# Kernel tuning notes

Hardware: AMD Instinct MI355X
Metric: run time of the kernel (lower is better)

The kernel has to match this reference:

```python
import math
import jax, jax.numpy as jnp
import numpy as np

B, S, D = 4, 2048, 1280
H, HD = 16, 80  # num_heads, head_dim
LOG2E = 1.442695041


def setup_inputs() -> dict:
    key = jax.random.key(0)
    ks = jax.random.split(key, 6)
    hidden_states = jax.random.normal(ks[0], (B, S, D), dtype=jnp.float32)
    # additive causal mask: 0 on/below diagonal, large negative above
    causal = jnp.tril(jnp.ones((S, S), dtype=bool))
    attention_mask = jnp.where(causal, 0.0, -1e9).astype(jnp.float32)[None, None, :, :]
    attention_mask = jnp.broadcast_to(attention_mask, (B, 1, S, S))
    scaling = jax.random.normal(ks[1], (HD,), dtype=jnp.float32)
    fan = 1.0 / math.sqrt(D)
    qkv_w = jax.random.normal(ks[2], (3 * H * HD, D), dtype=jnp.float32) * fan
    qkv_b = jax.random.normal(ks[3], (3 * H * HD,), dtype=jnp.float32) * fan
    o_w = jax.random.normal(ks[4], (D, H * HD), dtype=jnp.float32) * (1.0 / math.sqrt(H * HD))
    o_b = jax.random.normal(ks[5], (D,), dtype=jnp.float32) * fan
    return {
        "hidden_states": hidden_states,
        "attention_mask": attention_mask,
        "scaling": scaling,
        "qkv_w": qkv_w,
        "qkv_b": qkv_b,
        "o_w": o_w,
        "o_b": o_b,
    }


def reference(hidden_states, attention_mask, scaling, qkv_w, qkv_b, o_w, o_b):
    b, s, _ = hidden_states.shape
    qkv = hidden_states @ qkv_w.T + qkv_b  # [b, s, 3*H*HD]
    xq, xk, xv = jnp.split(qkv, [H * HD, 2 * H * HD], axis=-1)
    xq = xq.reshape(b, s, H, HD)
    xk = xk.reshape(b, s, H, HD)
    xv = xv.reshape(b, s, H, HD)
    # per-dim query scaling: softplus(scaling) * log2(e) / sqrt(head_dim)
    scale = jax.nn.softplus(scaling) * (LOG2E / math.sqrt(HD))
    xq = xq * scale[None, None, None, :]
    scores = jnp.einsum("bqhd,bkhd->bhqk", xq, xk) + attention_mask  # [b,H,s,s]
    probs = jax.nn.softmax(scores.astype(jnp.float32), axis=-1).astype(xq.dtype)
    out = jnp.einsum("bhqk,bkhd->bqhd", probs, xv).reshape(b, s, H * HD)
    return out @ o_w.T + o_b
```

## Files before the change

### kernel.cpp

```cpp
#include <hip/hip_runtime.h>
#include <math.h>

#define B_ 4
#define S_ 2048
#define D_ 1280
#define H_ 16
#define HD_ 80
#define HHD (H_ * HD_)
#define QKVN (3 * H_ * HD_)

typedef __bf16 bf16x8 __attribute__((ext_vector_type(8)));
typedef __bf16 bf16x4 __attribute__((ext_vector_type(4)));
typedef float  f32x4  __attribute__((ext_vector_type(4)));

__global__ __launch_bounds__(256) void cvt_bf16(
    const float* __restrict__ in, __bf16* __restrict__ out, int n8)
{
    const int i = blockIdx.x * 256 + threadIdx.x;
    if (i < n8) {
        const float4 a = ((const float4*)in)[2 * (size_t)i];
        const float4 b = ((const float4*)in)[2 * (size_t)i + 1];
        bf16x8 v = {(__bf16)a.x, (__bf16)a.y, (__bf16)a.z, (__bf16)a.w,
                    (__bf16)b.x, (__bf16)b.y, (__bf16)b.z, (__bf16)b.w};
        *(bf16x8*)(out + 8 * (size_t)i) = v;
    }
}

__device__ __forceinline__ void async_copy16(const void* g, void* l)
{
    __builtin_amdgcn_global_load_lds(
        (const __attribute__((address_space(1))) unsigned int*)g,
        (__attribute__((address_space(3))) unsigned int*)l, 16, 0, 0);
}

__device__ __forceinline__ void stage128x64(
    const __bf16* __restrict__ src, int K, char* lds, int tid)
{
    const int wave = tid >> 6, lane = tid & 63;
#pragma unroll
    for (int i = 0; i < 4; ++i) {
        const int c = (wave * 4 + i) * 64 + lane;
        const int r = c >> 3;
        const int g = (c & 7) ^ (r & 7);
        async_copy16(src + (size_t)r * K + g * 8, lds + (wave * 4 + i) * 1024);
    }
}

__device__ __forceinline__ bf16x8 frag_ld(const char* lds, int m, int j)
{
    return *(const bf16x8*)(lds + m * 128 + ((j ^ (m & 7)) << 4));
}

__device__ __forceinline__ void mfma_loop(
    const __bf16* __restrict__ A, const __bf16* __restrict__ W, int K,
    char* ldsA, char* ldsB, int tid, f32x4 acc[4][4])
{
    const int wave = tid >> 6;
    const int wm = wave >> 1, wn = wave & 1;
    const int l16 = tid & 15, quad = (tid & 63) >> 4;

#pragma unroll
    for (int mi = 0; mi < 4; ++mi)
#pragma unroll
        for (int ni = 0; ni < 4; ++ni) acc[mi][ni] = (f32x4){0.f, 0.f, 0.f, 0.f};

    for (int k0 = 0; k0 < K; k0 += 64) {
        __syncthreads();
        stage128x64(A + k0, K, ldsA, tid);
        stage128x64(W + k0, K, ldsB, tid);
        __syncthreads();
#pragma unroll
        for (int ks = 0; ks < 2; ++ks) {
            bf16x8 af[4], bfr[4];
#pragma unroll
            for (int mi = 0; mi < 4; ++mi)
                af[mi] = frag_ld(ldsA, wm * 64 + mi * 16 + l16, ks * 4 + quad);
#pragma unroll
            for (int ni = 0; ni < 4; ++ni)
                bfr[ni] = frag_ld(ldsB, wn * 64 + ni * 16 + l16, ks * 4 + quad);
#pragma unroll
            for (int mi = 0; mi < 4; ++mi)
#pragma unroll
                for (int ni = 0; ni < 4; ++ni)
                    acc[mi][ni] = __builtin_amdgcn_mfma_f32_16x16x32_bf16(
                        af[mi], bfr[ni], acc[mi][ni], 0, 0, 0);
        }
    }
}

__global__ __launch_bounds__(256) void gemm_qkv_mfma(
    const __bf16* __restrict__ Ab, const __bf16* __restrict__ Wb,
    const float* __restrict__ bias, const float* __restrict__ scaling,
    __bf16* __restrict__ Qb, __bf16* __restrict__ Kb, __bf16* __restrict__ Vtb)
{
    __shared__ __align__(16) char ldsA[128 * 128];
    __shared__ __align__(16) char ldsB[128 * 128];
    const int tid = threadIdx.x;
    const int m0 = blockIdx.y * 128, n0 = blockIdx.x * 128;

    f32x4 acc[4][4];
    mfma_loop(Ab + (size_t)m0 * D_, Wb + (size_t)n0 * D_, D_, ldsA, ldsB, tid, acc);

    const int wave = tid >> 6, wm = wave >> 1, wn = wave & 1;
    const int l16 = tid & 15, quad = (tid & 63) >> 4;
    const int sec = n0 / HHD;

#pragma unroll
    for (int ni = 0; ni < 4; ++ni) {
        const int col = n0 + wn * 64 + ni * 16 + l16;
        const int cis = col - sec * HHD;
        const int h = cis / HD_;
        const int d = cis - h * HD_;
        const float bv = bias[col];
        float qsv = 0.f;
        if (sec == 0)
            qsv = log1pf(expf(scaling[d])) *
                  (1.442695041f * 1.442695041f / 8.944271910f);
#pragma unroll
        for (int mi = 0; mi < 4; ++mi) {
#pragma unroll
            for (int r = 0; r < 4; ++r) {
                const int row = m0 + wm * 64 + mi * 16 + quad * 4 + r;
                const int bb = row >> 11;
                const int s = row & (S_ - 1);
                const size_t bh = (size_t)(bb * H_ + h);
                const float v = acc[mi][ni][r] + bv;
                if (sec == 0)      Qb[(bh * S_ + s) * HD_ + d] = (__bf16)(v * qsv);
                else if (sec == 1) Kb[(bh * S_ + s) * HD_ + d] = (__bf16)v;
                else               Vtb[(bh * HD_ + d) * S_ + s] = (__bf16)v;
            }
        }
    }
}

__global__ __launch_bounds__(256) void gemm_o_mfma(
    const __bf16* __restrict__ Ab, const __bf16* __restrict__ Wb,
    const float* __restrict__ bias, float* __restrict__ C)
{
    __shared__ __align__(16) char ldsA[128 * 128];
    __shared__ __align__(16) char ldsB[128 * 128];
    const int tid = threadIdx.x;
    const int m0 = blockIdx.y * 128, n0 = blockIdx.x * 128;

    f32x4 acc[4][4];
    mfma_loop(Ab + (size_t)m0 * D_, Wb + (size_t)n0 * D_, D_, ldsA, ldsB, tid, acc);

    const int wave = tid >> 6, wm = wave >> 1, wn = wave & 1;
    const int l16 = tid & 15, quad = (tid & 63) >> 4;

#pragma unroll
    for (int ni = 0; ni < 4; ++ni) {
        const int col = n0 + wn * 64 + ni * 16 + l16;
        const float bv = bias[col];
#pragma unroll
        for (int mi = 0; mi < 4; ++mi) {
#pragma unroll
            for (int r = 0; r < 4; ++r) {
                const int row = m0 + wm * 64 + mi * 16 + quad * 4 + r;
                C[(size_t)row * D_ + col] = acc[mi][ni][r] + bv;
            }
        }
    }
}

struct KF8 { bf16x8 f0, f1, f2; };

__device__ __forceinline__ void kload8(
    const __bf16* __restrict__ base, int row, int quad, KF8& kf)
{
    const __bf16* r = base + (size_t)row * HD_;
    kf.f0 = *(const bf16x8*)(r + quad * 8);
    kf.f1 = *(const bf16x8*)(r + 32 + quad * 8);
    bf16x8 z = {};
    if (quad < 2) z = *(const bf16x8*)(r + 64 + quad * 8);
    kf.f2 = z;
}

#define ATTN_BODY(KT, C0, C1, N0, N1)                                          \
    {                                                                          \
        const int k0 = (KT) * 32;                                              \
        const bool do_lo = ((KT) < nkt_lo);                  \
                     \
        bf16x8 vf0 = *(const bf16x8*)(Vbase + (size_t)( 0 + l16) * S_ + k0 + quad * 8); \
        bf16x8 vf1 = *(const bf16x8*)(Vbase + (size_t)(16 + l16) * S_ + k0 + quad * 8); \
        bf16x8 vf2 = *(const bf16x8*)(Vbase + (size_t)(32 + l16) * S_ + k0 + quad * 8); \
        bf16x8 vf3 = *(const bf16x8*)(Vbase + (size_t)(48 + l16) * S_ + k0 + quad * 8); \
        bf16x8 vf4 = *(const bf16x8*)(Vbase + (size_t)(64 + l16) * S_ + k0 + quad * 8); \
         \
        f32x4 sH0 = (f32x4){0.f,0.f,0.f,0.f}, sH1 = sH0, sL0 = sH0, sL1 = sH0; \
        __builtin_amdgcn_s_setprio(1);                                         \
        sH0 = __builtin_amdgcn_mfma_f32_16x16x32_bf16(C0.f0, qfH.f0, sH0, 0, 0, 0); \
        sH0 = __builtin_amdgcn_mfma_f32_16x16x32_bf16(C0.f1, qfH.f1, sH0, 0, 0, 0); \
        sH0 = __builtin_amdgcn_mfma_f32_16x16x32_bf16(C0.f2, qfH.f2, sH0, 0, 0, 0); \
        sH1 = __builtin_amdgcn_mfma_f32_16x16x32_bf16(C1.f0, qfH.f0, sH1, 0, 0, 0); \
        sH1 = __builtin_amdgcn_mfma_f32_16x16x32_bf16(C1.f1, qfH.f1, sH1, 0, 0, 0); \
        sH1 = __builtin_amdgcn_mfma_f32_16x16x32_bf16(C1.f2, qfH.f2, sH1, 0, 0, 0); \
        if (do_lo) {                                                           \
            sL0 = __builtin_amdgcn_mfma_f32_16x16x32_bf16(C0.f0, qfL.f0, sL0, 0, 0, 0); \
            sL0 = __builtin_amdgcn_mfma_f32_16x16x32_bf16(C0.f1, qfL.f1, sL0, 0, 0, 0); \
            sL0 = __builtin_amdgcn_mfma_f32_16x16x32_bf16(C0.f2, qfL.f2, sL0, 0, 0, 0); \
            sL1 = __builtin_amdgcn_mfma_f32_16x16x32_bf16(C1.f0, qfL.f0, sL1, 0, 0, 0); \
            sL1 = __builtin_amdgcn_mfma_f32_16x16x32_bf16(C1.f1, qfL.f1, sL1, 0, 0, 0); \
            sL1 = __builtin_amdgcn_mfma_f32_16x16x32_bf16(C1.f2, qfL.f2, sL1, 0, 0, 0); \
        }                                                                      \
        __builtin_amdgcn_s_setprio(0);                                         \
               \
        {                                                                      \
            const int kn = ((KT) + 1 < nkt_hi ? (KT) + 1 : (KT)) * 32;         \
            kload8(Kbase, kn + l16, quad, N0);                                 \
            kload8(Kbase, kn + 16 + l16, quad, N1);                            \
        }                                                                      \
                \
        float aH;                                                              \
        {                                                                      \
            if (k0 + 31 > q_hi) {                                              \
                _Pragma("unroll")                                              \
                for (int i = 0; i < 4; ++i) {                                  \
                    sH0[i] = (k0 + quad * 4 + i <= q_hi + l16) ? sH0[i] : -1e30f; \
                    sH1[i] = (k0 + 16 + quad * 4 + i <= q_hi + l16) ? sH1[i] : -1e30f; \
                }                                                              \
            }                                                                  \
            float m01 = fmaxf(sH0[0], sH0[1]);                                 \
            float m23 = fmaxf(sH0[2], sH0[3]);                                 \
            float m45 = fmaxf(sH1[0], sH1[1]);                                 \
            float m67 = fmaxf(sH1[2], sH1[3]);                                 \
            float mx = fmaxf(fmaxf(m01, m23), fmaxf(m45, m67));                \
            mx = fmaxf(mx, __shfl_xor(mx, 16));                                \
            mx = fmaxf(mx, __shfl_xor(mx, 32));                                \
            const float mn = fmaxf(mH, mx);                                    \
            aH = exp2f(mH - mn);                                               \
            mH = mn;                                                           \
            float rs = 0.f;                                                    \
            _Pragma("unroll")                                                  \
            for (int i = 0; i < 4; ++i) {                                      \
                const float p0 = exp2f(sH0[i] - mn);                           \
                const float p1 = exp2f(sH1[i] - mn);                           \
                sH0[i] = p0; sH1[i] = p1;                                      \
                rs += p0 + p1;                                                 \
            }                                                                  \
            lH = lH * aH + rs;                           \
            bf16x4 pk0 = {(__bf16)sH0[0], (__bf16)sH0[1],                      \
                          (__bf16)sH0[2], (__bf16)sH0[3]};                     \
            bf16x4 pk1 = {(__bf16)sH1[0], (__bf16)sH1[1],                      \
                          (__bf16)sH1[2], (__bf16)sH1[3]};                     \
            *(bf16x4*)&Ps[wave][0][l16][quad * 4] = pk0;                       \
            *(bf16x4*)&Ps[wave][0][l16][16 + quad * 4] = pk1;                  \
        }                                                                      \
                                          \
        float aL = 1.f;                                                        \
        if (do_lo) {                                                           \
            if (k0 + 31 > q_lo) {                                              \
                _Pragma("unroll")                                              \
                for (int i = 0; i < 4; ++i) {                                  \
                    sL0[i] = (k0 + quad * 4 + i <= q_lo + l16) ? sL0[i] : -1e30f; \
                    sL1[i] = (k0 + 16 + quad * 4 + i <= q_lo + l16) ? sL1[i] : -1e30f; \
                }                                                              \
            }                                                                  \
            float m01 = fmaxf(sL0[0], sL0[1]);                                 \
            float m23 = fmaxf(sL0[2], sL0[3]);                                 \
            float m45 = fmaxf(sL1[0], sL1[1]);                                 \
            float m67 = fmaxf(sL1[2], sL1[3]);                                 \
            float mx = fmaxf(fmaxf(m01, m23), fmaxf(m45, m67));                \
            mx = fmaxf(mx, __shfl_xor(mx, 16));                                \
            mx = fmaxf(mx, __shfl_xor(mx, 32));                                \
            const float mn = fmaxf(mL, mx);                                    \
            aL = exp2f(mL - mn);                                               \
            mL = mn;                                                           \
            float rs = 0.f;                                                    \
            _Pragma("unroll")                                                  \
            for (int i = 0; i < 4; ++i) {                                      \
                const float p0 = exp2f(sL0[i] - mn);                           \
                const float p1 = exp2f(sL1[i] - mn);                           \
                sL0[i] = p0; sL1[i] = p1;                                      \
                rs += p0 + p1;                                                 \
            }                                                                  \
            lL = lL * aL + rs;                                                 \
            bf16x4 pk0 = {(__bf16)sL0[0], (__bf16)sL0[1],                      \
                          (__bf16)sL0[2], (__bf16)sL0[3]};                     \
            bf16x4 pk1 = {(__bf16)sL1[0], (__bf16)sL1[1],                      \
                          (__bf16)sL1[2], (__bf16)sL1[3]};                     \
            *(bf16x4*)&Ps[wave][1][l16][quad * 4] = pk0;                       \
            *(bf16x4*)&Ps[wave][1][l16][16 + quad * 4] = pk1;                  \
        }                                                                      \
        asm volatile("s_waitcnt lgkmcnt(0)" ::: "memory");                     \
        const bf16x8 pfH = *(const bf16x8*)&Ps[wave][0][l16][quad * 8];        \
        const bf16x8 pfL = *(const bf16x8*)&Ps[wave][1][l16][quad * 8];        \
           \
        __builtin_amdgcn_s_setprio(1);                                         \
        {                                                                      \
            f32x4 c0, c1, c2, c3, c4;                                          \
            _Pragma("unroll")                                                  \
            for (int i = 0; i < 4; ++i) {                                      \
                c0[i] = oH0[i] * aH; c1[i] = oH1[i] * aH; c2[i] = oH2[i] * aH; \
                c3[i] = oH3[i] * aH; c4[i] = oH4[i] * aH;                      \
            }                                                                  \
            oH0 = __builtin_amdgcn_mfma_f32_16x16x32_bf16(vf0, pfH, c0, 0, 0, 0); \
            oH1 = __builtin_amdgcn_mfma_f32_16x16x32_bf16(vf1, pfH, c1, 0, 0, 0); \
            oH2 = __builtin_amdgcn_mfma_f32_16x16x32_bf16(vf2, pfH, c2, 0, 0, 0); \
            oH3 = __builtin_amdgcn_mfma_f32_16x16x32_bf16(vf3, pfH, c3, 0, 0, 0); \
            oH4 = __builtin_amdgcn_mfma_f32_16x16x32_bf16(vf4, pfH, c4, 0, 0, 0); \
        }                                                                      \
        if (do_lo) {                                                           \
            f32x4 c0, c1, c2, c3, c4;                                          \
            _Pragma("unroll")                                                  \
            for (int i = 0; i < 4; ++i) {                                      \
                c0[i] = oL0[i] * aL; c1[i] = oL1[i] * aL; c2[i] = oL2[i] * aL; \
                c3[i] = oL3[i] * aL; c4[i] = oL4[i] * aL;                      \
            }                                                                  \
            oL0 = __builtin_amdgcn_mfma_f32_16x16x32_bf16(vf0, pfL, c0, 0, 0, 0); \
            oL1 = __builtin_amdgcn_mfma_f32_16x16x32_bf16(vf1, pfL, c1, 0, 0, 0); \
            oL2 = __builtin_amdgcn_mfma_f32_16x16x32_bf16(vf2, pfL, c2, 0, 0, 0); \
            oL3 = __builtin_amdgcn_mfma_f32_16x16x32_bf16(vf3, pfL, c3, 0, 0, 0); \
            oL4 = __builtin_amdgcn_mfma_f32_16x16x32_bf16(vf4, pfL, c4, 0, 0, 0); \
        }                                                                      \
        __builtin_amdgcn_s_setprio(0);                                         \
    }

__global__ __launch_bounds__(256, 2) void attn_v11(
    const __bf16* __restrict__ Qb, const __bf16* __restrict__ Kb,
    const __bf16* __restrict__ Vtb, __bf16* __restrict__ out)
{
    __shared__ __align__(16) __bf16 Ps[4][2][16][40];

    const int tid = threadIdx.x;
    const int wave = tid >> 6;
    const int lane = tid & 63;
    const int l16 = lane & 15;
    const int quad = lane >> 4;

    const int flat = blockIdx.x;
    const int c = flat & 7;
    const int slot = flat >> 3;
    const int bhgrp = slot >> 4;
    const int xslot = slot & 15;
    const int bh = bhgrp * 8 + c;
    const int x = (xslot + 5 * bhgrp) & 15;
    const int b = bh >> 4, h = bh & 15;

    const int q_lo = 64 * x + 16 * wave;
    const int q_hi = 64 * (31 - x) + 16 * wave;

    const __bf16* Qbase = Qb + (size_t)bh * S_ * HD_;
    const __bf16* Kbase = Kb + (size_t)bh * S_ * HD_;
    const __bf16* Vbase = Vtb + (size_t)bh * HD_ * S_;

    KF8 qfL, qfH;
    kload8(Qbase, q_lo + l16, quad, qfL);
    kload8(Qbase, q_hi + l16, quad, qfH);

    float mL = -1e30f, lL = 0.f, mH = -1e30f, lH = 0.f;
    f32x4 oH0 = (f32x4){0.f,0.f,0.f,0.f}, oH1 = oH0, oH2 = oH0, oH3 = oH0, oH4 = oH0;
    f32x4 oL0 = oH0, oL1 = oH0, oL2 = oH0, oL3 = oH0, oL4 = oH0;

    const int nkt_lo = (q_lo + 16 + 31) >> 5;
    const int nkt_hi = (q_hi + 16 + 31) >> 5;

    KF8 kA0, kA1, kB0, kB1;
    kload8(Kbase, l16, quad, kA0);
    kload8(Kbase, 16 + l16, quad, kA1);

    int kt = 0;
    while (true) {
        ATTN_BODY(kt, kA0, kA1, kB0, kB1);
        if (++kt == nkt_hi) break;
        ATTN_BODY(kt, kB0, kB1, kA0, kA1);
        if (++kt == nkt_hi) break;
    }

    float lHs = lH + __shfl_xor(lH, 16);
    lHs += __shfl_xor(lHs, 32);
    float lLs = lL + __shfl_xor(lL, 16);
    lLs += __shfl_xor(lLs, 32);
    const float invH = 1.f / lHs;
    const float invL = 1.f / lLs;
    const size_t rowH = ((size_t)b * S_ + q_hi + l16) * HHD + h * HD_ + quad * 4;
    const size_t rowL = ((size_t)b * S_ + q_lo + l16) * HHD + h * HD_ + quad * 4;
    {
        bf16x4 v0 = {(__bf16)(oH0[0]*invH), (__bf16)(oH0[1]*invH), (__bf16)(oH0[2]*invH), (__bf16)(oH0[3]*invH)};
        bf16x4 v1 = {(__bf16)(oH1[0]*invH), (__bf16)(oH1[1]*invH), (__bf16)(oH1[2]*invH), (__bf16)(oH1[3]*invH)};
        bf16x4 v2 = {(__bf16)(oH2[0]*invH), (__bf16)(oH2[1]*invH), (__bf16)(oH2[2]*invH), (__bf16)(oH2[3]*invH)};
        bf16x4 v3 = {(__bf16)(oH3[0]*invH), (__bf16)(oH3[1]*invH), (__bf16)(oH3[2]*invH), (__bf16)(oH3[3]*invH)};
        bf16x4 v4 = {(__bf16)(oH4[0]*invH), (__bf16)(oH4[1]*invH), (__bf16)(oH4[2]*invH), (__bf16)(oH4[3]*invH)};
        *(bf16x4*)(out + rowH)      = v0;
        *(bf16x4*)(out + rowH + 16) = v1;
        *(bf16x4*)(out + rowH + 32) = v2;
        *(bf16x4*)(out + rowH + 48) = v3;
        *(bf16x4*)(out + rowH + 64) = v4;
    }
    {
        bf16x4 v0 = {(__bf16)(oL0[0]*invL), (__bf16)(oL0[1]*invL), (__bf16)(oL0[2]*invL), (__bf16)(oL0[3]*invL)};
        bf16x4 v1 = {(__bf16)(oL1[0]*invL), (__bf16)(oL1[1]*invL), (__bf16)(oL1[2]*invL), (__bf16)(oL1[3]*invL)};
        bf16x4 v2 = {(__bf16)(oL2[0]*invL), (__bf16)(oL2[1]*invL), (__bf16)(oL2[2]*invL), (__bf16)(oL2[3]*invL)};
        bf16x4 v3 = {(__bf16)(oL3[0]*invL), (__bf16)(oL3[1]*invL), (__bf16)(oL3[2]*invL), (__bf16)(oL3[3]*invL)};
        bf16x4 v4 = {(__bf16)(oL4[0]*invL), (__bf16)(oL4[1]*invL), (__bf16)(oL4[2]*invL), (__bf16)(oL4[3]*invL)};
        *(bf16x4*)(out + rowL)      = v0;
        *(bf16x4*)(out + rowL + 16) = v1;
        *(bf16x4*)(out + rowL + 32) = v2;
        *(bf16x4*)(out + rowL + 48) = v3;
        *(bf16x4*)(out + rowL + 64) = v4;
    }
}

extern "C" void kernel_launch(void* const* d_in, const int* in_sizes, int n_in,
                              void* d_out, int out_size, void* d_ws, size_t ws_size,
                              hipStream_t stream)
{
    const float* hidden  = (const float*)d_in[0];
    const float* scaling = (const float*)d_in[2];
    const float* qkv_w   = (const float*)d_in[3];
    const float* qkv_b   = (const float*)d_in[4];
    const float* o_w     = (const float*)d_in[5];
    const float* o_b     = (const float*)d_in[6];
    float* out = (float*)d_out;

    const size_t N_HID = (size_t)B_ * S_ * D_;
    const size_t N_QW  = (size_t)QKVN * D_;
    const size_t N_OW  = (size_t)D_ * D_;
    const size_t NPH   = (size_t)B_ * H_ * S_ * HD_;

    __bf16* Ab    = (__bf16*)d_ws;
    __bf16* Wqb   = Ab + N_HID;
    __bf16* Wob   = Wqb + N_QW;
    __bf16* Qb    = Wob + N_OW;
    __bf16* Kb    = Qb + NPH;
    __bf16* Vtb   = Kb + NPH;
    __bf16* attnb = Vtb + NPH;

    dim3 blk(256);

    cvt_bf16<<<dim3(N_HID / 8 / 256), blk, 0, stream>>>(hidden, Ab, N_HID / 8);
    cvt_bf16<<<dim3(N_QW  / 8 / 256), blk, 0, stream>>>(qkv_w, Wqb, N_QW / 8);
    cvt_bf16<<<dim3(N_OW  / 8 / 256), blk, 0, stream>>>(o_w,   Wob, N_OW / 8);

    gemm_qkv_mfma<<<dim3(QKVN / 128, B_ * S_ / 128), blk, 0, stream>>>(
        Ab, Wqb, qkv_b, scaling, Qb, Kb, Vtb);

    attn_v11<<<dim3(16 * H_ * B_), blk, 0, stream>>>(Qb, Kb, Vtb, attnb);

    gemm_o_mfma<<<dim3(D_ / 128, B_ * S_ / 128), blk, 0, stream>>>(
        attnb, Wob, o_b, out);
}
```

Baseline: 510.4 us.

## Widen attention key tile from 32 to 64 keys per iteration

The attention inner loop now processes 64 keys per step instead of 32. It issues four QK MFMA groups and two PV MFMA chains per step, and the shared P buffer gains a second 32-wide slice. Each softmax max/shuffle/rescale pass is now spread over twice as many keys, which halves the loop trip count and the online-softmax overhead per key. The cost is more live registers (extra K fragments, ten V fragments, eight score accumulators) at the occupancy-2 launch bound, a single-buffered K prefetch instead of ping-pong, and more wasted masked work on the diagonal tile.

```diff
diff --git a/kernel.cpp b/kernel.cpp
--- a/kernel.cpp
+++ b/kernel.cpp
@@ -176,55 +176,62 @@
     kf.f2 = z;
 }
 
-#define ATTN_BODY(KT, C0, C1, N0, N1)                                          \
+#define QK3(SREG, KF, QF)                                                      \
+    SREG = __builtin_amdgcn_mfma_f32_16x16x32_bf16(KF.f0, QF.f0, SREG, 0, 0, 0); \
+    SREG = __builtin_amdgcn_mfma_f32_16x16x32_bf16(KF.f1, QF.f1, SREG, 0, 0, 0); \
+    SREG = __builtin_amdgcn_mfma_f32_16x16x32_bf16(KF.f2, QF.f2, SREG, 0, 0, 0);
+
+#define MASK4(SREG, BASE, Q)                                                   \
+    _Pragma("unroll")                                                          \
+    for (int i = 0; i < 4; ++i)                                                \
+        SREG[i] = ((BASE) + quad * 4 + i <= (Q) + l16) ? SREG[i] : -1e30f;
+
+#define ATTN_BODY64(KT)                                                        \
     {                                                                          \
-        const int k0 = (KT) * 32;                                              \
+        const int k0 = (KT) * 64;                                              \
         const bool do_lo = ((KT) < nkt_lo);                  \
-                     \
-        bf16x8 vf0 = *(const bf16x8*)(Vbase + (size_t)( 0 + l16) * S_ + k0 + quad * 8); \
-        bf16x8 vf1 = *(const bf16x8*)(Vbase + (size_t)(16 + l16) * S_ + k0 + quad * 8); \
-        bf16x8 vf2 = *(const bf16x8*)(Vbase + (size_t)(32 + l16) * S_ + k0 + quad * 8); \
-        bf16x8 vf3 = *(const bf16x8*)(Vbase + (size_t)(48 + l16) * S_ + k0 + quad * 8); \
-        bf16x8 vf4 = *(const bf16x8*)(Vbase + (size_t)(64 + l16) * S_ + k0 + quad * 8); \
          \
-        f32x4 sH0 = (f32x4){0.f,0.f,0.f,0.f}, sH1 = sH0, sL0 = sH0, sL1 = sH0; \
+        const bf16x8 vf00 = *(const bf16x8*)(Vbase + (size_t)( 0 + l16) * S_ + k0 + quad * 8);      \
+        const bf16x8 vf01 = *(const bf16x8*)(Vbase + (size_t)( 0 + l16) * S_ + k0 + 32 + quad * 8); \
+        const bf16x8 vf10 = *(const bf16x8*)(Vbase + (size_t)(16 + l16) * S_ + k0 + quad * 8);      \
+        const bf16x8 vf11 = *(const bf16x8*)(Vbase + (size_t)(16 + l16) * S_ + k0 + 32 + quad * 8); \
+        const bf16x8 vf20 = *(const bf16x8*)(Vbase + (size_t)(32 + l16) * S_ + k0 + quad * 8);      \
+        const bf16x8 vf21 = *(const bf16x8*)(Vbase + (size_t)(32 + l16) * S_ + k0 + 32 + quad * 8); \
+        const bf16x8 vf30 = *(const bf16x8*)(Vbase + (size_t)(48 + l16) * S_ + k0 + quad * 8);      \
+        const bf16x8 vf31 = *(const bf16x8*)(Vbase + (size_t)(48 + l16) * S_ + k0 + 32 + quad * 8); \
+        const bf16x8 vf40 = *(const bf16x8*)(Vbase + (size_t)(64 + l16) * S_ + k0 + quad * 8);      \
+        const bf16x8 vf41 = *(const bf16x8*)(Vbase + (size_t)(64 + l16) * S_ + k0 + 32 + quad * 8); \
+                          \
+        f32x4 sH0 = (f32x4){0.f,0.f,0.f,0.f}, sH1 = sH0, sH2 = sH0, sH3 = sH0; \
+        f32x4 sL0 = sH0, sL1 = sH0, sL2 = sH0, sL3 = sH0;                      \
         __builtin_amdgcn_s_setprio(1);                                         \
-        sH0 = __builtin_amdgcn_mfma_f32_16x16x32_bf16(C0.f0, qfH.f0, sH0, 0, 0, 0); \
-        sH0 = __builtin_amdgcn_mfma_f32_16x16x32_bf16(C0.f1, qfH.f1, sH0, 0, 0, 0); \
-        sH0 = __builtin_amdgcn_mfma_f32_16x16x32_bf16(C0.f2, qfH.f2, sH0, 0, 0, 0); \
-        sH1 = __builtin_amdgcn_mfma_f32_16x16x32_bf16(C1.f0, qfH.f0, sH1, 0, 0, 0); \
-        sH1 = __builtin_amdgcn_mfma_f32_16x16x32_bf16(C1.f1, qfH.f1, sH1, 0, 0, 0); \
-        sH1 = __builtin_amdgcn_mfma_f32_16x16x32_bf16(C1.f2, qfH.f2, sH1, 0, 0, 0); \
+        QK3(sH0, kf0, qfH) QK3(sH1, kf1, qfH) QK3(sH2, kf2, qfH) QK3(sH3, kf3, qfH) \
         if (do_lo) {                                                           \
-            sL0 = __builtin_amdgcn_mfma_f32_16x16x32_bf16(C0.f0, qfL.f0, sL0, 0, 0, 0); \
-            sL0 = __builtin_amdgcn_mfma_f32_16x16x32_bf16(C0.f1, qfL.f1, sL0, 0, 0, 0); \
-            sL0 = __builtin_amdgcn_mfma_f32_16x16x32_bf16(C0.f2, qfL.f2, sL0, 0, 0, 0); \
-            sL1 = __builtin_amdgcn_mfma_f32_16x16x32_bf16(C1.f0, qfL.f0, sL1, 0, 0, 0); \
-            sL1 = __builtin_amdgcn_mfma_f32_16x16x32_bf16(C1.f1, qfL.f1, sL1, 0, 0, 0); \
-            sL1 = __builtin_amdgcn_mfma_f32_16x16x32_bf16(C1.f2, qfL.f2, sL1, 0, 0, 0); \
+            QK3(sL0, kf0, qfL) QK3(sL1, kf1, qfL)                              \
+            QK3(sL2, kf2, qfL) QK3(sL3, kf3, qfL)                              \
         }                                                                      \
         __builtin_amdgcn_s_setprio(0);                                         \
-               \
+         \
+         \
         {                                                                      \
-            const int kn = ((KT) + 1 < nkt_hi ? (KT) + 1 : (KT)) * 32;         \
-            kload8(Kbase, kn + l16, quad, N0);                                 \
-            kload8(Kbase, kn + 16 + l16, quad, N1);                            \
+            const int kn = ((KT) + 1 < nkt_hi ? (KT) + 1 : (KT)) * 64;         \
+            kload8(Kbase, kn + l16, quad, kf0);                                \
+            kload8(Kbase, kn + 16 + l16, quad, kf1);                           \
+            kload8(Kbase, kn + 32 + l16, quad, kf2);                           \
+            kload8(Kbase, kn + 48 + l16, quad, kf3);                           \
         }                                                                      \
                 \
         float aH;                                                              \
         {                                                                      \
-            if (k0 + 31 > q_hi) {                                              \
-                _Pragma("unroll")                                              \
-                for (int i = 0; i < 4; ++i) {                                  \
-                    sH0[i] = (k0 + quad * 4 + i <= q_hi + l16) ? sH0[i] : -1e30f; \
-                    sH1[i] = (k0 + 16 + quad * 4 + i <= q_hi + l16) ? sH1[i] : -1e30f; \
-                }                                                              \
-            }                                                                  \
-            float m01 = fmaxf(sH0[0], sH0[1]);                                 \
-            float m23 = fmaxf(sH0[2], sH0[3]);                                 \
-            float m45 = fmaxf(sH1[0], sH1[1]);                                 \
-            float m67 = fmaxf(sH1[2], sH1[3]);                                 \
-            float mx = fmaxf(fmaxf(m01, m23), fmaxf(m45, m67));                \
+            if (k0 + 63 > q_hi) {                                              \
+                MASK4(sH0, k0, q_hi)      MASK4(sH1, k0 + 16, q_hi)            \
+                MASK4(sH2, k0 + 32, q_hi) MASK4(sH3, k0 + 48, q_hi)            \
+            }                                                                  \
+            float mA = fmaxf(fmaxf(sH0[0], sH0[1]), fmaxf(sH0[2], sH0[3]));    \
+            float mB = fmaxf(fmaxf(sH1[0], sH1[1]), fmaxf(sH1[2], sH1[3]));    \
+            float mC = fmaxf(fmaxf(sH2[0], sH2[1]), fmaxf(sH2[2], sH2[3]));    \
+            float mD = fmaxf(fmaxf(sH3[0], sH3[1]), fmaxf(sH3[2], sH3[3]));    \
+            float mx = fmaxf(fmaxf(mA, mB), fmaxf(mC, mD));                    \
             mx = fmaxf(mx, __shfl_xor(mx, 16));                                \
             mx = fmaxf(mx, __shfl_xor(mx, 32));                                \
             const float mn = fmaxf(mH, mx);                                    \
@@ -235,32 +242,33 @@
             for (int i = 0; i < 4; ++i) {                                      \
                 const float p0 = exp2f(sH0[i] - mn);                           \
                 const float p1 = exp2f(sH1[i] - mn);                           \
-                sH0[i] = p0; sH1[i] = p1;                                      \
-                rs += p0 + p1;                                                 \
+                const float p2 = exp2f(sH2[i] - mn);                           \
+                const float p3 = exp2f(sH3[i] - mn);                           \
+                sH0[i] = p0; sH1[i] = p1; sH2[i] = p2; sH3[i] = p3;            \
+                rs += (p0 + p1) + (p2 + p3);                                   \
             }                                                                  \
             lH = lH * aH + rs;                           \
-            bf16x4 pk0 = {(__bf16)sH0[0], (__bf16)sH0[1],                      \
-                          (__bf16)sH0[2], (__bf16)sH0[3]};                     \
-            bf16x4 pk1 = {(__bf16)sH1[0], (__bf16)sH1[1],                      \
-                          (__bf16)sH1[2], (__bf16)sH1[3]};                     \
-            *(bf16x4*)&Ps[wave][0][l16][quad * 4] = pk0;                       \
-            *(bf16x4*)&Ps[wave][0][l16][16 + quad * 4] = pk1;                  \
+            *(bf16x4*)&Ps[wave][0][l16][0][quad * 4] =                         \
+                (bf16x4){(__bf16)sH0[0], (__bf16)sH0[1], (__bf16)sH0[2], (__bf16)sH0[3]}; \
+            *(bf16x4*)&Ps[wave][0][l16][0][16 + quad * 4] =                    \
+                (bf16x4){(__bf16)sH1[0], (__bf16)sH1[1], (__bf16)sH1[2], (__bf16)sH1[3]}; \
+            *(bf16x4*)&Ps[wave][0][l16][1][quad * 4] =                         \
+                (bf16x4){(__bf16)sH2[0], (__bf16)sH2[1], (__bf16)sH2[2], (__bf16)sH2[3]}; \
+            *(bf16x4*)&Ps[wave][0][l16][1][16 + quad * 4] =                    \
+                (bf16x4){(__bf16)sH3[0], (__bf16)sH3[1], (__bf16)sH3[2], (__bf16)sH3[3]}; \
         }                                                                      \
                                           \
         float aL = 1.f;                                                        \
         if (do_lo) {                                                           \
-            if (k0 + 31 > q_lo) {                                              \
-                _Pragma("unroll")                                              \
-                for (int i = 0; i < 4; ++i) {                                  \
-                    sL0[i] = (k0 + quad * 4 + i <= q_lo + l16) ? sL0[i] : -1e30f; \
-                    sL1[i] = (k0 + 16 + quad * 4 + i <= q_lo + l16) ? sL1[i] : -1e30f; \
-                }                                                              \
-            }                                                                  \
-            float m01 = fmaxf(sL0[0], sL0[1]);                                 \
-            float m23 = fmaxf(sL0[2], sL0[3]);                                 \
-            float m45 = fmaxf(sL1[0], sL1[1]);                                 \
-            float m67 = fmaxf(sL1[2], sL1[3]);                                 \
-            float mx = fmaxf(fmaxf(m01, m23), fmaxf(m45, m67));                \
+            if (k0 + 63 > q_lo) {                                              \
+                MASK4(sL0, k0, q_lo)      MASK4(sL1, k0 + 16, q_lo)            \
+                MASK4(sL2, k0 + 32, q_lo) MASK4(sL3, k0 + 48, q_lo)            \
+            }                                                                  \
+            float mA = fmaxf(fmaxf(sL0[0], sL0[1]), fmaxf(sL0[2], sL0[3]));    \
+            float mB = fmaxf(fmaxf(sL1[0], sL1[1]), fmaxf(sL1[2], sL1[3]));    \
+            float mC = fmaxf(fmaxf(sL2[0], sL2[1]), fmaxf(sL2[2], sL2[3]));    \
+            float mD = fmaxf(fmaxf(sL3[0], sL3[1]), fmaxf(sL3[2], sL3[3]));    \
+            float mx = fmaxf(fmaxf(mA, mB), fmaxf(mC, mD));                    \
             mx = fmaxf(mx, __shfl_xor(mx, 16));                                \
             mx = fmaxf(mx, __shfl_xor(mx, 32));                                \
             const float mn = fmaxf(mL, mx);                                    \
@@ -271,21 +279,27 @@
             for (int i = 0; i < 4; ++i) {                                      \
                 const float p0 = exp2f(sL0[i] - mn);                           \
                 const float p1 = exp2f(sL1[i] - mn);                           \
-                sL0[i] = p0; sL1[i] = p1;                                      \
-                rs += p0 + p1;                                                 \
+                const float p2 = exp2f(sL2[i] - mn);                           \
+                const float p3 = exp2f(sL3[i] - mn);                           \
+                sL0[i] = p0; sL1[i] = p1; sL2[i] = p2; sL3[i] = p3;            \
+                rs += (p0 + p1) + (p2 + p3);                                   \
             }                                                                  \
             lL = lL * aL + rs;                                                 \
-            bf16x4 pk0 = {(__bf16)sL0[0], (__bf16)sL0[1],                      \
-                          (__bf16)sL0[2], (__bf16)sL0[3]};                     \
-            bf16x4 pk1 = {(__bf16)sL1[0], (__bf16)sL1[1],                      \
-                          (__bf16)sL1[2], (__bf16)sL1[3]};                     \
-            *(bf16x4*)&Ps[wave][1][l16][quad * 4] = pk0;                       \
-            *(bf16x4*)&Ps[wave][1][l16][16 + quad * 4] = pk1;                  \
+            *(bf16x4*)&Ps[wave][1][l16][0][quad * 4] =                         \
+                (bf16x4){(__bf16)sL0[0], (__bf16)sL0[1], (__bf16)sL0[2], (__bf16)sL0[3]}; \
+            *(bf16x4*)&Ps[wave][1][l16][0][16 + quad * 4] =                    \
+                (bf16x4){(__bf16)sL1[0], (__bf16)sL1[1], (__bf16)sL1[2], (__bf16)sL1[3]}; \
+            *(bf16x4*)&Ps[wave][1][l16][1][quad * 4] =                         \
+                (bf16x4){(__bf16)sL2[0], (__bf16)sL2[1], (__bf16)sL2[2], (__bf16)sL2[3]}; \
+            *(bf16x4*)&Ps[wave][1][l16][1][16 + quad * 4] =                    \
+                (bf16x4){(__bf16)sL3[0], (__bf16)sL3[1], (__bf16)sL3[2], (__bf16)sL3[3]}; \
         }                                                                      \
         asm volatile("s_waitcnt lgkmcnt(0)" ::: "memory");                     \
-        const bf16x8 pfH = *(const bf16x8*)&Ps[wave][0][l16][quad * 8];        \
-        const bf16x8 pfL = *(const bf16x8*)&Ps[wave][1][l16][quad * 8];        \
-           \
+        const bf16x8 pfH0 = *(const bf16x8*)&Ps[wave][0][l16][0][quad * 8];    \
+        const bf16x8 pfH1 = *(const bf16x8*)&Ps[wave][0][l16][1][quad * 8];    \
+        const bf16x8 pfL0 = *(const bf16x8*)&Ps[wave][1][l16][0][quad * 8];    \
+        const bf16x8 pfL1 = *(const bf16x8*)&Ps[wave][1][l16][1][quad * 8];    \
+         \
         __builtin_amdgcn_s_setprio(1);                                         \
         {                                                                      \
             f32x4 c0, c1, c2, c3, c4;                                          \
@@ -294,11 +308,16 @@
                 c0[i] = oH0[i] * aH; c1[i] = oH1[i] * aH; c2[i] = oH2[i] * aH; \
                 c3[i] = oH3[i] * aH; c4[i] = oH4[i] * aH;                      \
             }                                                                  \
-            oH0 = __builtin_amdgcn_mfma_f32_16x16x32_bf16(vf0, pfH, c0, 0, 0, 0); \
-            oH1 = __builtin_amdgcn_mfma_f32_16x16x32_bf16(vf1, pfH, c1, 0, 0, 0); \
-            oH2 = __builtin_amdgcn_mfma_f32_16x16x32_bf16(vf2, pfH, c2, 0, 0, 0); \
-            oH3 = __builtin_amdgcn_mfma_f32_16x16x32_bf16(vf3, pfH, c3, 0, 0, 0); \
-            oH4 = __builtin_amdgcn_mfma_f32_16x16x32_bf16(vf4, pfH, c4, 0, 0, 0); \
+            oH0 = __builtin_amdgcn_mfma_f32_16x16x32_bf16(vf00, pfH0, c0, 0, 0, 0); \
+            oH1 = __builtin_amdgcn_mfma_f32_16x16x32_bf16(vf10, pfH0, c1, 0, 0, 0); \
+            oH2 = __builtin_amdgcn_mfma_f32_16x16x32_bf16(vf20, pfH0, c2, 0, 0, 0); \
+            oH3 = __builtin_amdgcn_mfma_f32_16x16x32_bf16(vf30, pfH0, c3, 0, 0, 0); \
+            oH4 = __builtin_amdgcn_mfma_f32_16x16x32_bf16(vf40, pfH0, c4, 0, 0, 0); \
+            oH0 = __builtin_amdgcn_mfma_f32_16x16x32_bf16(vf01, pfH1, oH0, 0, 0, 0); \
+            oH1 = __builtin_amdgcn_mfma_f32_16x16x32_bf16(vf11, pfH1, oH1, 0, 0, 0); \
+            oH2 = __builtin_amdgcn_mfma_f32_16x16x32_bf16(vf21, pfH1, oH2, 0, 0, 0); \
+            oH3 = __builtin_amdgcn_mfma_f32_16x16x32_bf16(vf31, pfH1, oH3, 0, 0, 0); \
+            oH4 = __builtin_amdgcn_mfma_f32_16x16x32_bf16(vf41, pfH1, oH4, 0, 0, 0); \
         }                                                                      \
         if (do_lo) {                                                           \
             f32x4 c0, c1, c2, c3, c4;                                          \
@@ -307,20 +326,25 @@
                 c0[i] = oL0[i] * aL; c1[i] = oL1[i] * aL; c2[i] = oL2[i] * aL; \
                 c3[i] = oL3[i] * aL; c4[i] = oL4[i] * aL;                      \
             }                                                                  \
-            oL0 = __builtin_amdgcn_mfma_f32_16x16x32_bf16(vf0, pfL, c0, 0, 0, 0); \
-            oL1 = __builtin_amdgcn_mfma_f32_16x16x32_bf16(vf1, pfL, c1, 0, 0, 0); \
-            oL2 = __builtin_amdgcn_mfma_f32_16x16x32_bf16(vf2, pfL, c2, 0, 0, 0); \
-            oL3 = __builtin_amdgcn_mfma_f32_16x16x32_bf16(vf3, pfL, c3, 0, 0, 0); \
-            oL4 = __builtin_amdgcn_mfma_f32_16x16x32_bf16(vf4, pfL, c4, 0, 0, 0); \
+            oL0 = __builtin_amdgcn_mfma_f32_16x16x32_bf16(vf00, pfL0, c0, 0, 0, 0); \
+            oL1 = __builtin_amdgcn_mfma_f32_16x16x32_bf16(vf10, pfL0, c1, 0, 0, 0); \
+            oL2 = __builtin_amdgcn_mfma_f32_16x16x32_bf16(vf20, pfL0, c2, 0, 0, 0); \
+            oL3 = __builtin_amdgcn_mfma_f32_16x16x32_bf16(vf30, pfL0, c3, 0, 0, 0); \
+            oL4 = __builtin_amdgcn_mfma_f32_16x16x32_bf16(vf40, pfL0, c4, 0, 0, 0); \
+            oL0 = __builtin_amdgcn_mfma_f32_16x16x32_bf16(vf01, pfL1, oL0, 0, 0, 0); \
+            oL1 = __builtin_amdgcn_mfma_f32_16x16x32_bf16(vf11, pfL1, oL1, 0, 0, 0); \
+            oL2 = __builtin_amdgcn_mfma_f32_16x16x32_bf16(vf21, pfL1, oL2, 0, 0, 0); \
+            oL3 = __builtin_amdgcn_mfma_f32_16x16x32_bf16(vf31, pfL1, oL3, 0, 0, 0); \
+            oL4 = __builtin_amdgcn_mfma_f32_16x16x32_bf16(vf41, pfL1, oL4, 0, 0, 0); \
         }                                                                      \
         __builtin_amdgcn_s_setprio(0);                                         \
     }
 
-__global__ __launch_bounds__(256, 2) void attn_v11(
+__global__ __launch_bounds__(256, 2) void attn_v13(
     const __bf16* __restrict__ Qb, const __bf16* __restrict__ Kb,
     const __bf16* __restrict__ Vtb, __bf16* __restrict__ out)
 {
-    __shared__ __align__(16) __bf16 Ps[4][2][16][40];
+    __shared__ __align__(16) __bf16 Ps[4][2][16][2][40];
 
     const int tid = threadIdx.x;
     const int wave = tid >> 6;
@@ -352,19 +376,17 @@
     f32x4 oH0 = (f32x4){0.f,0.f,0.f,0.f}, oH1 = oH0, oH2 = oH0, oH3 = oH0, oH4 = oH0;
     f32x4 oL0 = oH0, oL1 = oH0, oL2 = oH0, oL3 = oH0, oL4 = oH0;
 
-    const int nkt_lo = (q_lo + 16 + 31) >> 5;
-    const int nkt_hi = (q_hi + 16 + 31) >> 5;
-
-    KF8 kA0, kA1, kB0, kB1;
-    kload8(Kbase, l16, quad, kA0);
-    kload8(Kbase, 16 + l16, quad, kA1);
-
-    int kt = 0;
-    while (true) {
-        ATTN_BODY(kt, kA0, kA1, kB0, kB1);
-        if (++kt == nkt_hi) break;
-        ATTN_BODY(kt, kB0, kB1, kA0, kA1);
-        if (++kt == nkt_hi) break;
+    const int nkt_lo = (q_lo + 16 + 63) >> 6;
+    const int nkt_hi = (q_hi + 16 + 63) >> 6;
+
+    KF8 kf0, kf1, kf2, kf3;
+    kload8(Kbase, l16, quad, kf0);
+    kload8(Kbase, 16 + l16, quad, kf1);
+    kload8(Kbase, 32 + l16, quad, kf2);
+    kload8(Kbase, 48 + l16, quad, kf3);
+
+    for (int kt = 0; kt < nkt_hi; ++kt) {
+        ATTN_BODY64(kt);
     }
 
     float lHs = lH + __shfl_xor(lH, 16);
@@ -435,7 +457,7 @@
     gemm_qkv_mfma<<<dim3(QKVN / 128, B_ * S_ / 128), blk, 0, stream>>>(
         Ab, Wqb, qkv_b, scaling, Qb, Kb, Vtb);
 
-    attn_v11<<<dim3(16 * H_ * B_), blk, 0, stream>>>(Qb, Kb, Vtb, attnb);
+    attn_v13<<<dim3(16 * H_ * B_), blk, 0, stream>>>(Qb, Kb, Vtb, attnb);
 
     gemm_o_mfma<<<dim3(D_ / 128, B_ * S_ / 128), blk, 0, stream>>>(
         attnb, Wob, o_b, out);
```

Measured after the change: 503.3 us. Within noise of the previous version (-1.4%).
